# Optimization experiments

Measured on AMD Instinct MI355X. Metric: run time of the kernel, lower is better.

Reference implementation:

```python
import jax, jax.numpy as jnp
import numpy as np
from jax import lax

T, K, F = 262144, 20, 16


def setup_inputs() -> dict:
    key = jax.random.key(0)
    k1, k2, k3, k4 = jax.random.split(key, 4)
    return {
        "observations": jax.random.normal(k1, (T, F), dtype=jnp.float32),
        "beta_logits": jax.random.normal(k2, (K,), dtype=jnp.float32),
        "pi_logits": jax.random.normal(k3, (K, K), dtype=jnp.float32),
        "means": jax.random.normal(k4, (K, F), dtype=jnp.float32),
        "log_vars": jnp.zeros((K, F), dtype=jnp.float32),
    }


def _stick_breaking(logits):
    b = jax.nn.sigmoid(logits)
    cp = jnp.cumprod(1.0 - b)
    return b * jnp.concatenate([jnp.ones((1,), logits.dtype), cp[:-1]])


def _emission_logp(obs, means, log_vars):
    # Diagonal-covariance MultivariateNormal log_prob, vectorized over T and K
    # without materializing a [T,K,F] intermediate.
    var = jnp.exp(log_vars) + 1e-6                       # [K,F]
    inv = 1.0 / var
    const = jnp.sum(means * means * inv + jnp.log(2.0 * jnp.pi * var), axis=1)  # [K]
    quad = (obs * obs) @ inv.T - 2.0 * (obs @ (means * inv).T)                  # [T,K]
    return -0.5 * (quad + const[None, :])


def reference(observations, beta_logits, pi_logits, means, log_vars):
    w = _stick_breaking(beta_logits)                      # [K]
    P = jax.nn.softmax(pi_logits, axis=1)                 # [K,K]
    em = _emission_logp(observations, means, log_vars)    # [T,K]

    # Forward recursion (normalized alpha, as in the original)
    a0 = w * jnp.exp(em[0])
    a0 = a0 / (a0.sum() + 1e-10)

    def fstep(a, e):
        x = (a @ P) * jnp.exp(e)
        x = x / (x.sum() + 1e-10)
        return x, x

    _, a_rest = lax.scan(fstep, a0, em[1:])
    alpha = jnp.concatenate([a0[None], a_rest], axis=0)   # [T,K]

    # Backward recursion (normalized beta)
    bT = jnp.ones((K,), observations.dtype)

    def bstep(bn, e):
        x = P @ (bn * jnp.exp(e))
        x = x / (x.sum() + 1e-10)
        return x, x

    _, b_rest = lax.scan(bstep, bT, em[1:], reverse=True)
    beta = jnp.concatenate([b_rest, bT[None]], axis=0)    # [T,K]

    log_likelihood = jnp.log(alpha[-1].sum() + 1e-10)
    return alpha, beta, log_likelihood
```

## Files before the change

### kernel.cpp

```cpp
#include <hip/hip_runtime.h>


namespace {
constexpr int Tn = 262144;
constexpr int Kn = 20;
constexpr int Fn = 16;
constexpr float EPSF = 1e-10f;
constexpr float TINY = 1e-35f;

constexpr int Ln3 = 32;
constexpr int Wn3 = 20;
constexpr int NC3 = Tn / Ln3;
constexpr int NBF = NC3 / 16;
constexpr int NBS3 = NC3 / 4;

constexpr size_t OFF_P    = 0;
constexpr size_t OFF_W    = 400;
constexpr size_t OFF_CK   = 420;
constexpr size_t OFF_MVIV = 440;
constexpr size_t OFF_E    = 1152;
constexpr size_t OFF_MF   = OFF_E + (size_t)Tn*20 + 64;
constexpr size_t OFF_MB   = OFF_MF + (size_t)Tn;
constexpr size_t OFF_MATF = OFF_MB + (size_t)Tn;
constexpr size_t OFF_MATB = OFF_MATF + 4*(size_t)NC3;
constexpr size_t OFF_SF   = OFF_MATB + 4*(size_t)NC3;
constexpr size_t OFF_SB   = OFF_SF + NC3;
constexpr size_t OFF_END  = OFF_SB + NC3;
}

#if __has_builtin(__builtin_amdgcn_rcpf)
#define FRCP(x) __builtin_amdgcn_rcpf(x)
#else
#define FRCP(x) (1.0f/(x))
#endif

template<int CTRL>
__device__ __forceinline__ float dpp_add(float v) {
  int s = __builtin_amdgcn_update_dpp(0, __float_as_int(v), CTRL, 0xF, 0xF, true);
  return v + __int_as_float(s);
}

__device__ __forceinline__ float reduce16(float v) {
  v = dpp_add<0xB1>(v);
  v = dpp_add<0x4E>(v);
  v = dpp_add<0x141>(v);
  v = dpp_add<0x140>(v);
  return v;
}

__global__ __launch_bounds__(64) void prep_kernel(
    const float* beta_logits, const float* pi_logits,
    const float* means, const float* log_vars, float* ws)
{
  int k = threadIdx.x;
  if (k < Kn) {
    float row[Kn];
    float mx = -1e30f;
#pragma unroll
    for (int j = 0; j < Kn; ++j) { row[j] = pi_logits[k*Kn + j]; mx = fmaxf(mx, row[j]); }
    float s = 0.f;
#pragma unroll
    for (int j = 0; j < Kn; ++j) { row[j] = expf(row[j] - mx); s += row[j]; }
    float invs = 1.0f / s;
#pragma unroll
    for (int j = 0; j < Kn; ++j) ws[OFF_P + k*Kn + j] = row[j] * invs;
    float ck = 0.f;
#pragma unroll
    for (int f = 0; f < Fn; ++f) {
      float lv  = log_vars[k*Fn + f];
      float var = expf(lv) + 1e-6f;
      float iv  = 1.0f / var;
      float mu  = means[k*Fn + f];
      ((float2*)(ws + OFF_MVIV))[k*Fn + f] = make_float2(mu * iv, iv);
      ck += mu*mu*iv + logf(6.2831853071795864f * var);
    }
    ws[OFF_CK + k] = ck;
  } else if (k == Kn) {
    float cp = 1.f;
#pragma unroll
    for (int i = 0; i < Kn; ++i) {
      float b = 1.0f / (1.0f + expf(-beta_logits[i]));
      ws[OFF_W + i] = b * cp;
      cp *= (1.0f - b);
    }
  }
}

__global__ __launch_bounds__(320) void emis_kernel(const float* __restrict__ obs, float* ws)
{
  __shared__ __align__(16) float so[64][20];
  __shared__ __align__(16) float scm[16][24];
  __shared__ __align__(16) float scv[16][24];
  __shared__ __align__(16) float sck[20];
  const int tid = threadIdx.x;
  const int t0 = blockIdx.x * 64;

  if (tid < 256) {
    float4 v = ((const float4*)(obs + (size_t)t0 * Fn))[tid];
    int r = tid >> 2, j = tid & 3;
    *(float4*)&so[r][j*4] = v;
  } else {
    int i = tid - 256;
#pragma unroll
    for (int q = 0; q < 5; ++q) {
      int idx = i * 5 + q;
      float2 c2 = ((const float2*)(ws + OFF_MVIV))[idx];
      int k = idx >> 4, f = idx & 15;
      scm[f][k] = c2.x;
      scv[f][k] = c2.y;
    }
    if (i < Kn) sck[i] = ws[OFF_CK + i];
  }
  __syncthreads();

  const int tl = tid / 5;
  const int k0 = (tid - tl*5) * 4;

  float o[16];
  *(float4*)&o[0]  = *(const float4*)&so[tl][0];
  *(float4*)&o[4]  = *(const float4*)&so[tl][4];
  *(float4*)&o[8]  = *(const float4*)&so[tl][8];
  *(float4*)&o[12] = *(const float4*)&so[tl][12];

  float s1x=0.f,s1y=0.f,s1z=0.f,s1w=0.f;
  float s2x=0.f,s2y=0.f,s2z=0.f,s2w=0.f;
#pragma unroll
  for (int f = 0; f < Fn; ++f) {
    float4 cm = *(const float4*)&scm[f][k0];
    float4 cv = *(const float4*)&scv[f][k0];
    float ov = o[f];
    s1x = fmaf(cv.x * ov, ov, s1x); s2x = fmaf(cm.x, ov, s2x);
    s1y = fmaf(cv.y * ov, ov, s1y); s2y = fmaf(cm.y, ov, s2y);
    s1z = fmaf(cv.z * ov, ov, s1z); s2z = fmaf(cm.z, ov, s2z);
    s1w = fmaf(cv.w * ov, ov, s1w); s2w = fmaf(cm.w, ov, s2w);
  }
  float4 ckv = *(const float4*)&sck[k0];
  float4 rr;
  rr.x = __expf(fmaf(-0.5f, s1x + ckv.x, s2x));
  rr.y = __expf(fmaf(-0.5f, s1y + ckv.y, s2y));
  rr.z = __expf(fmaf(-0.5f, s1z + ckv.z, s2z));
  rr.w = __expf(fmaf(-0.5f, s1w + ckv.w, s2w));
  *(float4*)(ws + OFF_E + (size_t)(t0 + tl)*20 + k0) = rr;
}

__global__ __launch_bounds__(256, 4) void scan3_kernel(float* ws, float* out)
{
  __shared__ __align__(16) float xsh[16][20];
  const int tid = threadIdx.x;
  const int g   = tid >> 4;
  const int ll  = tid & 15;
  const bool hi = (ll < 4);
  const int l4  = 16 + (ll & 3);
  const bool isF = ((int)blockIdx.x < NBF);
  const int c = (isF ? (int)blockIdx.x : (int)blockIdx.x - NBF) * 16 + g;
  const float* E = ws + OFF_E;
  float* xg = &xsh[g][0];

  float Pv0[Kn], Pv1[Kn];
#pragma unroll
  for (int k = 0; k < Kn; ++k) {
    if (isF) {
      Pv0[k] = ws[OFF_P + k*Kn + ll];
      float p1 = ws[OFF_P + k*Kn + l4];
      Pv1[k] = hi ? p1 : 0.f;
    } else {
      Pv0[k] = ws[OFF_P + ll*Kn + k];
      float p1 = ws[OFF_P + l4*Kn + k];
      Pv1[k] = hi ? p1 : 0.f;
    }
  }

  float Ma = 1.f, Mc = 0.f, Md = 1.f;
  float* mArr = ws + (isF ? OFF_MF : OFF_MB);
  float* uOut = out + (isF ? (size_t)0 : (size_t)Tn * Kn);

  auto mobius = [&](float m) {
    float na = m * Ma;
    float nc = fmaf(EPSF, Mc, na);
    float nd = EPSF * Md;
    float mx = fmaxf(nc, nd);
    float lam = (mx > 0.f) ? FRCP(mx) : 1.0f;
    Ma = na*lam; Mc = nc*lam; Md = nd*lam;
  };
  auto matvec2 = [&](float& r0, float& r1) {
    float xv[20];
    *(float4*)&xv[0]  = *(const float4*)&xg[0];
    *(float4*)&xv[4]  = *(const float4*)&xg[4];
    *(float4*)&xv[8]  = *(const float4*)&xg[8];
    *(float4*)&xv[12] = *(const float4*)&xg[12];
    *(float4*)&xv[16] = *(const float4*)&xg[16];
    float A0 = xv[0]*Pv0[0], A1 = xv[1]*Pv0[1];
    float B0 = xv[0]*Pv1[0], B1 = xv[1]*Pv1[1];
#pragma unroll
    for (int k = 2; k < 20; k += 2) {
      A0 = fmaf(xv[k],   Pv0[k],   A0);
      A1 = fmaf(xv[k+1], Pv0[k+1], A1);
      B0 = fmaf(xv[k],   Pv1[k],   B0);
      B1 = fmaf(xv[k+1], Pv1[k+1], B1);
    }
    r0 = A0 + A1; r1 = B0 + B1;
  };

  if (isF) {
    const int bodyStart = c * Ln3;
    const int tend = bodyStart + Ln3 - 1;
    const int t0 = (c == 0) ? 0 : (bodyStart - Wn3);
    float e0a = E[t0*20 + ll],     e1a = E[t0*20 + l4];
    float v0, v1;
    if (c == 0) {
      v0 = ws[OFF_W + ll] * e0a;
      v1 = hi ? ws[OFF_W + l4] * e1a : 0.f;
    } else {
      v0 = 0.05f * e0a;
      v1 = hi ? 0.05f * e1a : 0.f;
    }
    float sv = reduce16(v0 + v1);
    float m = sv;
    float iV = (sv > TINY) ? FRCP(sv) : 1.0f;
    if (sv <= TINY) { v0 = 0.05f; v1 = hi ? 0.05f : 0.f; }
    if (c == 0) {
      if (ll == 0) mArr[0] = m;
      mobius(m);
      uOut[ll] = v0 * iV;
      if (hi) uOut[l4] = v1 * iV;
    }
    float A = m * iV;
    float rho = (m > TINY) ? FRCP(m) : 1.0f;
    float e0b = E[(t0+1)*20 + ll], e1b = E[(t0+1)*20 + l4];
    float e0c = E[(t0+2)*20 + ll], e1c = E[(t0+2)*20 + l4];

#define FWD_STEP(REC)                                                     \
    {                                                                     \
      xg[ll] = v0;                                                        \
      if (hi) xg[16 + ll] = v1;                                           \
      float acc0, acc1; matvec2(acc0, acc1);                              \
      float er0 = e0a * rho, er1 = e1a * rho;                             \
      e0a = e0b; e0b = e0c; e0c = E[(t+3)*20 + ll];                       \
      e1a = e1b; e1b = e1c; e1c = E[(t+3)*20 + l4];                       \
      v0 = acc0 * er0; v1 = acc1 * er1;                                   \
      float sv2 = reduce16(v0 + v1);                                      \
      float mn = sv2 * A;                                                 \
      float iVn = (sv2 > TINY) ? FRCP(sv2) : 1.0f;                        \
      if (sv2 <= TINY) { v0 = 0.05f; v1 = hi ? 0.05f : 0.f; }             \
      if (REC) {                                                          \
        if (ll == 0) mArr[t] = mn;                                        \
        mobius(mn);                                                       \
        uOut[(size_t)t*Kn + ll] = v0 * iVn;                               \
        if (hi) uOut[(size_t)t*Kn + 16 + ll] = v1 * iVn;                  \
      }                                                                   \
      A = mn * iVn;                                                       \
      rho = (mn > TINY) ? FRCP(mn) : 1.0f;                                \
    }

    for (int t = t0 + 1; t < bodyStart; ++t) FWD_STEP(false)
    const int bstart2 = (c == 0) ? 1 : bodyStart;
    for (int t = bstart2; t <= tend; ++t) FWD_STEP(true)
#undef FWD_STEP
    if (ll == 0) ((float4*)(ws + OFF_MATF))[c] = make_float4(Ma, Mc, Md, 0.f);
  } else {
    const int bodyStart = c * Ln3;
    const int top = bodyStart + Ln3 - 1;
    int r0 = top + Wn3; if (r0 > Tn - 1) r0 = Tn - 1;
    float v0 = 0.05f, v1 = hi ? 0.05f : 0.f;
    float sv = reduce16(v0 + v1);
    float iV = (sv > TINY) ? FRCP(sv) : 1.0f;
    float A = iV;
    float rho = 1.0f;
    float e0a = E[r0*20 + ll],     e1a = E[r0*20 + l4];
    float e0b = E[(r0-1)*20 + ll], e1b = E[(r0-1)*20 + l4];
    float e0c = E[(r0-2)*20 + ll], e1c = E[(r0-2)*20 + l4];

#define BWD_STEP(REC)                                                     \
    {                                                                     \
      xg[ll] = v0 * e0a;                                                  \
      if (hi) xg[16 + ll] = v1 * e1a;                                     \
      float acc0, acc1; matvec2(acc0, acc1);                              \
      v0 = acc0 * rho; v1 = acc1 * rho;                                   \
      e0a = e0b; e0b = e0c; e0c = E[(r-2)*20 + ll];                       \
      e1a = e1b; e1b = e1c; e1c = E[(r-2)*20 + l4];                       \
      float sv2 = reduce16(v0 + v1);                                      \
      float mn = sv2 * A;                                                 \
      float iVn = (sv2 > TINY) ? FRCP(sv2) : 1.0f;                        \
      if (sv2 <= TINY) { v0 = 0.05f; v1 = hi ? 0.05f : 0.f; }             \
      if (REC) {                                                          \
        if (ll == 0) mArr[r+1] = mn;                                      \
        mobius(mn);                                                       \
        uOut[(size_t)r*Kn + ll] = v0 * iVn;                               \
        if (hi) uOut[(size_t)r*Kn + 16 + ll] = v1 * iVn;                  \
      }                                                                   \
      A = mn * iVn;                                                       \
      rho = (mn > TINY) ? FRCP(mn) : 1.0f;                                \
    }

    for (int r = r0 - 1; r > top; --r) BWD_STEP(false)
    int rb = (r0 - 1 < top) ? (r0 - 1) : top;
    for (int r = rb; r >= bodyStart; --r) BWD_STEP(true)
#undef BWD_STEP
    if (ll == 0) ((float4*)(ws + OFF_MATB))[NC3 - 1 - c] = make_float4(Ma, Mc, Md, 0.f);
  }
}

__global__ __launch_bounds__(1024) void combine4_kernel(float* ws, float* out)
{
  __shared__ float wag[16][3];
  __shared__ float wpre[16][3];
  const bool isF = (blockIdx.x == 0);
  const float4* M4 = (const float4*)(ws + (isF ? OFF_MATF : OFF_MATB));
  float* sArr = ws + (isF ? OFF_SF : OFF_SB);
  const float s0 = isF ? 1.0f : 20.0f;
  constexpr int PG = NC3 / 1024;
  const int tid  = threadIdx.x;
  const int lane = tid & 63;
  const int wid  = tid >> 6;

  float4 mm[PG];
#pragma unroll
  for (int i = 0; i < PG; ++i) mm[i] = M4[tid*PG + i];

  float a = 1.f, cc = 0.f, d = 1.f;
#pragma unroll
  for (int i = 0; i < PG; ++i) {
    float na = mm[i].x * a;
    float nc = fmaf(mm[i].y, a, mm[i].z * cc);
    float nd = mm[i].z * d;
    float mx = fmaxf(na, fmaxf(nc, nd));
    float lam = (mx > 0.f) ? FRCP(mx) : 1.0f;
    a = na*lam; cc = nc*lam; d = nd*lam;
  }

  float ia = a, ic = cc, id = d;
  for (int off = 1; off < 64; off <<= 1) {
    float pa = __shfl_up(ia, off, 64);
    float pc = __shfl_up(ic, off, 64);
    float pd = __shfl_up(id, off, 64);
    if (lane >= off) {
      float na = ia * pa;
      float nc = fmaf(ic, pa, id * pc);
      float nd = id * pd;
      float mx = fmaxf(na, fmaxf(nc, nd));
      float lam = (mx > 0.f) ? FRCP(mx) : 1.0f;
      ia = na*lam; ic = nc*lam; id = nd*lam;
    }
  }
  if (lane == 63) { wag[wid][0] = ia; wag[wid][1] = ic; wag[wid][2] = id; }
  __syncthreads();

  if (tid == 0) {
    float ea = 1.f, ec = 0.f, ed = 1.f;
#pragma unroll
    for (int w = 0; w < 16; ++w) {
      wpre[w][0] = ea; wpre[w][1] = ec; wpre[w][2] = ed;
      float na = wag[w][0] * ea;
      float nc = fmaf(wag[w][1], ea, wag[w][2] * ec);
      float nd = wag[w][2] * ed;
      float mx = fmaxf(na, fmaxf(nc, nd));
      float lam = (mx > 0.f) ? FRCP(mx) : 1.0f;
      ea = na*lam; ec = nc*lam; ed = nd*lam;
    }
    if (isF) {
      float den = fmaf(ec, s0, ed);
      float sfin = (den > 0.f) ? (ea * s0)/den : 0.f;
      out[(size_t)2 * Tn * Kn] = logf(sfin + EPSF);
    }
  }
  __syncthreads();

  float ea = __shfl_up(ia, 1, 64);
  float ec = __shfl_up(ic, 1, 64);
  float ed = __shfl_up(id, 1, 64);
  if (lane == 0) { ea = 1.f; ec = 0.f; ed = 1.f; }
  float pa = wpre[wid][0], pc = wpre[wid][1], pd = wpre[wid][2];
  float xa = ea * pa;
  float xc = fmaf(ec, pa, ed * pc);
  float xd = ed * pd;

  float num = xa * s0, den = fmaf(xc, s0, xd);
  float s = (den > 0.f) ? num/den : 0.f;
#pragma unroll
  for (int i = 0; i < PG; ++i) {
    sArr[tid*PG + i] = s;
    float nn = mm[i].x * s, dd = fmaf(mm[i].y, s, mm[i].z);
    s = (dd > 0.f) ? nn/dd : 0.f;
  }
}

__global__ __launch_bounds__(128) void scale3_kernel(float* ws, float* out)
{
  __shared__ float sig[4][Ln3];
  const int tid = threadIdx.x;
  const int g   = tid >> 5;
  const int jj  = tid & 31;
  const bool isF = ((int)blockIdx.x < NBS3);
  const int c = (isF ? (int)blockIdx.x : (int)blockIdx.x - NBS3) * 4 + g;
  constexpr int QPC = Ln3 * Kn / 4;

  if (isF) {
    const float* mArr = ws + OFF_MF;
    float s = ws[OFF_SF + c];
    const int t0 = c * Ln3;
    for (int i = 0; i < Ln3; ++i) {
      float mm = mArr[t0 + i];
      float z = s * mm;
      float sn = z * FRCP(z + EPSF);
      if (jj == 0) sig[g][i] = sn;
      s = sn;
    }
    __syncthreads();
    float4* A4 = (float4*)out + (size_t)c * QPC;
#pragma unroll
    for (int i = jj; i < QPC; i += 32) {
      int tl = i / 5;
      float sg = sig[g][tl];
      float4 v = A4[i];
      v.x *= sg; v.y *= sg; v.z *= sg; v.w *= sg;
      A4[i] = v;
    }
  } else {
    const float* mArr = ws + OFF_MB;
    const int slot = NC3 - 1 - c;
    float s = ws[OFF_SB + slot];
    const int bodyStart = c * Ln3;
    const int top = bodyStart + Ln3 - 1;
    const bool lastChunk = (c == NC3 - 1);
    for (int r = top; r >= bodyStart; --r) {
      if (r == Tn - 1) {
        if (jj == 0) sig[g][Ln3 - 1] = 1.0f;
        continue;
      }
      float mm = mArr[r + 1];
      float z = s * mm;
      float sn = z * FRCP(z + EPSF);
      if (jj == 0) sig[g][r - bodyStart] = sn;
      s = sn;
    }
    __syncthreads();
    float4* B4 = (float4*)out + ((size_t)Tn * Kn) / 4 + (size_t)c * QPC;
#pragma unroll
    for (int i = jj; i < QPC; i += 32) {
      int tl = i / 5;
      if (lastChunk && tl == Ln3 - 1) {
        B4[i] = make_float4(1.f, 1.f, 1.f, 1.f);
      } else {
        float sg = sig[g][tl];
        float4 v = B4[i];
        v.x *= sg; v.y *= sg; v.z *= sg; v.w *= sg;
        B4[i] = v;
      }
    }
  }
}

extern "C" void kernel_launch(void* const* d_in, const int* in_sizes, int n_in,
                              void* d_out, int out_size, void* d_ws, size_t ws_size,
                              hipStream_t stream) {
  const float* obs         = (const float*)d_in[0];
  const float* beta_logits = (const float*)d_in[1];
  const float* pi_logits   = (const float*)d_in[2];
  const float* means       = (const float*)d_in[3];
  const float* log_vars    = (const float*)d_in[4];
  float* out = (float*)d_out;
  float* ws  = (float*)d_ws;

  hipLaunchKernelGGL(prep_kernel, dim3(1), dim3(64), 0, stream,
                     beta_logits, pi_logits, means, log_vars, ws);
  hipLaunchKernelGGL(emis_kernel, dim3(Tn/64), dim3(320), 0, stream, obs, ws);
  hipLaunchKernelGGL(scan3_kernel, dim3(2*NBF), dim3(256), 0, stream, ws, out);
  hipLaunchKernelGGL(combine4_kernel, dim3(2), dim3(1024), 0, stream, ws, out);
  hipLaunchKernelGGL(scale3_kernel, dim3(2*NBS3), dim3(128), 0, stream, ws, out);
}
```

Measured before the change: 90.53 us.

## Store intermediate scan outputs as fp16 in-place and halve scan chunk length

The scan kernel now writes its per-chunk normalized alpha/beta values as packed half-precision into the first half of each chunk's output region. The scale kernel then reads those halves and expands them to scaled fp32 in place. The intent is to cut the bytes written and re-read between the two passes. Chunk length drops from 32 to 16, which doubles parallelism but also doubles the warm-up overhead per chunk, and the occupancy hint is dropped. Storing intermediates in fp16 loses precision and may exceed the output tolerance.

```diff
diff --git a/kernel.cpp b/kernel.cpp
--- a/kernel.cpp
+++ b/kernel.cpp
@@ -1,4 +1,5 @@
 #include <hip/hip_runtime.h>
+#include <hip/hip_fp16.h>
 
 
 namespace {
@@ -8,11 +9,12 @@
 constexpr float EPSF = 1e-10f;
 constexpr float TINY = 1e-35f;
 
-constexpr int Ln3 = 32;
+constexpr int Ln3 = 16;
 constexpr int Wn3 = 20;
 constexpr int NC3 = Tn / Ln3;
 constexpr int NBF = NC3 / 16;
 constexpr int NBS3 = NC3 / 4;
+constexpr int SPC = Ln3 * Kn;
 
 constexpr size_t OFF_P    = 0;
 constexpr size_t OFF_W    = 400;
@@ -143,7 +145,7 @@
   *(float4*)(ws + OFF_E + (size_t)(t0 + tl)*20 + k0) = rr;
 }
 
-__global__ __launch_bounds__(256, 4) void scan3_kernel(float* ws, float* out)
+__global__ __launch_bounds__(256) void scan3_kernel(float* ws, float* out)
 {
   __shared__ __align__(16) float xsh[16][20];
   const int tid = threadIdx.x;
@@ -172,7 +174,7 @@
 
   float Ma = 1.f, Mc = 0.f, Md = 1.f;
   float* mArr = ws + (isF ? OFF_MF : OFF_MB);
-  float* uOut = out + (isF ? (size_t)0 : (size_t)Tn * Kn);
+  __half* uH = (__half*)(out + (isF ? (size_t)0 : (size_t)Tn * Kn) + (size_t)c * SPC);
 
   auto mobius = [&](float m) {
     float na = m * Ma;
@@ -221,8 +223,8 @@
     if (c == 0) {
       if (ll == 0) mArr[0] = m;
       mobius(m);
-      uOut[ll] = v0 * iV;
-      if (hi) uOut[l4] = v1 * iV;
+      uH[ll] = __float2half(v0 * iV);
+      if (hi) uH[l4] = __float2half(v1 * iV);
     }
     float A = m * iV;
     float rho = (m > TINY) ? FRCP(m) : 1.0f;
@@ -245,8 +247,9 @@
       if (REC) {                                                          \
         if (ll == 0) mArr[t] = mn;                                        \
         mobius(mn);                                                       \
-        uOut[(size_t)t*Kn + ll] = v0 * iVn;                               \
-        if (hi) uOut[(size_t)t*Kn + 16 + ll] = v1 * iVn;                  \
+        int lt = t - bodyStart;                                           \
+        uH[lt*Kn + ll] = __float2half(v0 * iVn);                          \
+        if (hi) uH[lt*Kn + 16 + ll] = __float2half(v1 * iVn);             \
       }                                                                   \
       A = mn * iVn;                                                       \
       rho = (mn > TINY) ? FRCP(mn) : 1.0f;                                \
@@ -285,8 +288,9 @@
       if (REC) {                                                          \
         if (ll == 0) mArr[r+1] = mn;                                      \
         mobius(mn);                                                       \
-        uOut[(size_t)r*Kn + ll] = v0 * iVn;                               \
-        if (hi) uOut[(size_t)r*Kn + 16 + ll] = v1 * iVn;                  \
+        int lr = r - bodyStart;                                           \
+        uH[lr*Kn + ll] = __float2half(v0 * iVn);                          \
+        if (hi) uH[lr*Kn + 16 + ll] = __float2half(v1 * iVn);             \
       }                                                                   \
       A = mn * iVn;                                                       \
       rho = (mn > TINY) ? FRCP(mn) : 1.0f;                                \
@@ -392,12 +396,14 @@
   const int jj  = tid & 31;
   const bool isF = ((int)blockIdx.x < NBS3);
   const int c = (isF ? (int)blockIdx.x : (int)blockIdx.x - NBS3) * 4 + g;
-  constexpr int QPC = Ln3 * Kn / 4;
+  float* base = out + (isF ? (size_t)0 : (size_t)Tn * Kn) + (size_t)c * SPC;
+  const __half* hp = (const __half*)base;
 
   if (isF) {
     const float* mArr = ws + OFF_MF;
     float s = ws[OFF_SF + c];
     const int t0 = c * Ln3;
+#pragma unroll
     for (int i = 0; i < Ln3; ++i) {
       float mm = mArr[t0 + i];
       float z = s * mm;
@@ -405,23 +411,13 @@
       if (jj == 0) sig[g][i] = sn;
       s = sn;
     }
-    __syncthreads();
-    float4* A4 = (float4*)out + (size_t)c * QPC;
-#pragma unroll
-    for (int i = jj; i < QPC; i += 32) {
-      int tl = i / 5;
-      float sg = sig[g][tl];
-      float4 v = A4[i];
-      v.x *= sg; v.y *= sg; v.z *= sg; v.w *= sg;
-      A4[i] = v;
-    }
   } else {
     const float* mArr = ws + OFF_MB;
     const int slot = NC3 - 1 - c;
     float s = ws[OFF_SB + slot];
     const int bodyStart = c * Ln3;
     const int top = bodyStart + Ln3 - 1;
-    const bool lastChunk = (c == NC3 - 1);
+#pragma unroll
     for (int r = top; r >= bodyStart; --r) {
       if (r == Tn - 1) {
         if (jj == 0) sig[g][Ln3 - 1] = 1.0f;
@@ -433,20 +429,20 @@
       if (jj == 0) sig[g][r - bodyStart] = sn;
       s = sn;
     }
-    __syncthreads();
-    float4* B4 = (float4*)out + ((size_t)Tn * Kn) / 4 + (size_t)c * QPC;
-#pragma unroll
-    for (int i = jj; i < QPC; i += 32) {
-      int tl = i / 5;
-      if (lastChunk && tl == Ln3 - 1) {
-        B4[i] = make_float4(1.f, 1.f, 1.f, 1.f);
-      } else {
-        float sg = sig[g][tl];
-        float4 v = B4[i];
-        v.x *= sg; v.y *= sg; v.z *= sg; v.w *= sg;
-        B4[i] = v;
-      }
-    }
+  }
+
+  float vals[10];
+#pragma unroll
+  for (int q = 0; q < 10; ++q) vals[q] = __half2float(hp[jj*10 + q]);
+  __syncthreads();
+
+  const int tl = jj >> 1;
+  float sg = sig[g][tl];
+  const bool onesRow = (!isF && c == NC3 - 1 && tl == Ln3 - 1);
+#pragma unroll
+  for (int q = 0; q < 10; ++q) {
+    float vv = onesRow ? 1.0f : vals[q] * sg;
+    base[jj*10 + q] = vv;
   }
 }
 
```

Result: slower. 107.8 us (+19.0%).
